# Performance work log

Measured on AMD Instinct MI355X. Metric: run time of the kernel, lower is better.

Reference implementation:

```python
import jax, jax.numpy as jnp
import numpy as np

B, S, D, MAX_CLS = 128, 512, 768, 64


def setup_inputs() -> dict:
    key = jax.random.key(0)
    k1, k2 = jax.random.split(key)
    encoded_output = jax.random.normal(k1, (B, S, D), dtype=jnp.float32)
    W = jax.random.normal(k2, (D, 1), dtype=jnp.float32) * 0.02
    b = jnp.zeros((1,), dtype=jnp.float32)
    # Build cls_idx with a variable number of CLS positions per row;
    # row 0 gets exactly MAX_CLS so the batch max equals MAX_CLS (matches
    # the original data-dependent max(cls_idx.sum(dim=1))).
    rng = np.random.default_rng(0)
    cls = np.zeros((B, S), dtype=bool)
    counts = rng.integers(8, MAX_CLS + 1, size=B)
    counts[0] = MAX_CLS
    for i in range(B):
        pos = rng.choice(S, size=counts[i], replace=False)
        cls[i, pos] = True
    cls_idx = jnp.asarray(cls)
    return {"encoded_output": encoded_output, "W": W, "b": b,
            "cls_idx": cls_idx, "max_num_cls": MAX_CLS}


def reference(encoded_output, W, b, cls_idx, max_num_cls):
    # extract_cls_embeddings: mask, ragged-gather CLS rows, pad to max count.
    maskf = cls_idx[..., None].astype(encoded_output.dtype)  # [B,S,1]
    masked = encoded_output * maskf                          # [B,S,D]
    # stable argsort puts True (CLS) positions first, preserving order
    order = jnp.argsort(jnp.logical_not(cls_idx), axis=1, stable=True)  # [B,S]
    idx = order[:, :max_num_cls]                             # [B,M]
    gathered = jnp.take_along_axis(masked, idx[..., None], axis=1)  # [B,M,D]
    counts = jnp.sum(cls_idx, axis=1)                        # [B]
    valid = jnp.arange(max_num_cls)[None, :] < counts[:, None]  # [B,M]
    gathered = gathered * valid[..., None].astype(gathered.dtype)  # zero-pad
    # LinearClassifier: linear + sigmoid
    logits = jax.nn.sigmoid(jnp.einsum('bmd,dk->bmk', gathered, W) + b)
    return logits
```

## Files before the change

### kernel.cpp

```cpp
#include <hip/hip_runtime.h>
#include <math.h>

#define B_  128
#define S_  512
#define D_  768
#define M_  64

__global__ void Summarizer_pos_kernel(const int* __restrict__ cls,
                                      int* __restrict__ pos,
                                      int* __restrict__ cnt) {
    const int b    = blockIdx.x;
    const int lane = threadIdx.x;
    const int* row = cls + (size_t)b * S_;

    int base = 0;
    #pragma unroll
    for (int i = 0; i < S_ / 64; ++i) {
        const int v = row[i * 64 + lane];
        const unsigned long long mask = __ballot(v != 0);
        const unsigned long long below = (lane == 0) ? 0ull
                                        : (mask & ((1ull << lane) - 1ull));
        const int rank = base + __popcll(below);
        if (v != 0 && rank < M_) {
            pos[(size_t)b * M_ + rank] = i * 64 + lane;
        }
        base += __popcll(mask);
    }
    if (lane == 0) cnt[b] = (base < M_) ? base : M_;
}

__global__ void Summarizer_dot_kernel(const float* __restrict__ enc,
                                      const float* __restrict__ W,
                                      const float* __restrict__ bias,
                                      const int* __restrict__ pos,
                                      const int* __restrict__ cnt,
                                      float* __restrict__ out) {
    const int tid  = blockIdx.x * blockDim.x + threadIdx.x;
    const int wid  = tid >> 6;
    const int lane = tid & 63;
    const int b    = wid >> 6;
    const int m    = wid & (M_ - 1);

    float sum = 0.0f;
    const int count = cnt[b];
    if (m < count) {
        const int p = pos[(size_t)b * M_ + m];
        const float4* row4 = (const float4*)(enc + ((size_t)b * S_ + p) * D_);
        const float4* w4   = (const float4*)W;

        const float4 r0 = row4[lane];
        const float4 r1 = row4[lane + 64];
        const float4 r2 = row4[lane + 128];
        const float4 w0 = w4[lane];
        const float4 w1 = w4[lane + 64];
        const float4 w2 = w4[lane + 128];

        sum = r0.x * w0.x + r0.y * w0.y + r0.z * w0.z + r0.w * w0.w
            + r1.x * w1.x + r1.y * w1.y + r1.z * w1.z + r1.w * w1.w
            + r2.x * w2.x + r2.y * w2.y + r2.z * w2.z + r2.w * w2.w;
    }

    #pragma unroll
    for (int off = 32; off > 0; off >>= 1) {
        sum += __shfl_down(sum, off, 64);
    }

    if (lane == 0) {
        const float x = sum + bias[0];
        out[wid] = 1.0f / (1.0f + __expf(-x));
    }
}

extern "C" void kernel_launch(void* const* d_in, const int* in_sizes, int n_in,
                              void* d_out, int out_size, void* d_ws, size_t ws_size,
                              hipStream_t stream) {
    const float* enc  = (const float*)d_in[0];
    const float* W    = (const float*)d_in[1];
    const float* bias = (const float*)d_in[2];
    const int*   cls  = (const int*)d_in[3];
    float* out = (float*)d_out;

    int* pos = (int*)d_ws;
    int* cnt = pos + (size_t)B_ * M_;

    Summarizer_pos_kernel<<<B_, 64, 0, stream>>>(cls, pos, cnt);

    const int total_threads = B_ * M_ * 64;
    Summarizer_dot_kernel<<<total_threads / 256, 256, 0, stream>>>(
        enc, W, bias, pos, cnt, out);
}
```

Baseline: 242.7 us.

## Fuse CLS position scan and dot-product into one kernel

```diff
diff --git a/kernel.cpp b/kernel.cpp
--- a/kernel.cpp
+++ b/kernel.cpp
@@ -6,68 +6,67 @@
 #define D_  768
 #define M_  64
 
-__global__ void Summarizer_pos_kernel(const int* __restrict__ cls,
-                                      int* __restrict__ pos,
-                                      int* __restrict__ cnt) {
-    const int b    = blockIdx.x;
-    const int lane = threadIdx.x;
-    const int* row = cls + (size_t)b * S_;
+__global__ __launch_bounds__(256) void Summarizer_fused_kernel(
+    const float* __restrict__ enc,
+    const float* __restrict__ W,
+    const float* __restrict__ bias,
+    const int*   __restrict__ cls,
+    float*       __restrict__ out) {
 
-    int base = 0;
-    #pragma unroll
-    for (int i = 0; i < S_ / 64; ++i) {
-        const int v = row[i * 64 + lane];
-        const unsigned long long mask = __ballot(v != 0);
-        const unsigned long long below = (lane == 0) ? 0ull
-                                        : (mask & ((1ull << lane) - 1ull));
-        const int rank = base + __popcll(below);
-        if (v != 0 && rank < M_) {
-            pos[(size_t)b * M_ + rank] = i * 64 + lane;
+    __shared__ int s_pos[M_];
+    __shared__ int s_cnt;
+
+    const int tid  = threadIdx.x;
+    const int lane = tid & 63;
+    const int wave = tid >> 6;
+    const int b    = blockIdx.x >> 1;
+    const int half = blockIdx.x & 1;
+
+    if (wave == 0) {
+        const int* row = cls + (size_t)b * S_;
+        int base = 0;
+        #pragma unroll
+        for (int i = 0; i < S_ / 64; ++i) {
+            const int v = row[i * 64 + lane];
+            const unsigned long long mask  = __ballot(v != 0);
+            const unsigned long long below = mask & ((1ull << lane) - 1ull);
+            const int rank = base + __popcll(below);
+            if (v != 0 && rank < M_) s_pos[rank] = i * 64 + lane;
+            base += __popcll(mask);
         }
-        base += __popcll(mask);
-    }
-    if (lane == 0) cnt[b] = (base < M_) ? base : M_;
-}
-
-__global__ void Summarizer_dot_kernel(const float* __restrict__ enc,
-                                      const float* __restrict__ W,
-                                      const float* __restrict__ bias,
-                                      const int* __restrict__ pos,
-                                      const int* __restrict__ cnt,
-                                      float* __restrict__ out) {
-    const int tid  = blockIdx.x * blockDim.x + threadIdx.x;
-    const int wid  = tid >> 6;
-    const int lane = tid & 63;
-    const int b    = wid >> 6;
-    const int m    = wid & (M_ - 1);
-
-    float sum = 0.0f;
-    const int count = cnt[b];
-    if (m < count) {
-        const int p = pos[(size_t)b * M_ + m];
-        const float4* row4 = (const float4*)(enc + ((size_t)b * S_ + p) * D_);
-        const float4* w4   = (const float4*)W;
-
-        const float4 r0 = row4[lane];
-        const float4 r1 = row4[lane + 64];
-        const float4 r2 = row4[lane + 128];
-        const float4 w0 = w4[lane];
-        const float4 w1 = w4[lane + 64];
-        const float4 w2 = w4[lane + 128];
-
-        sum = r0.x * w0.x + r0.y * w0.y + r0.z * w0.z + r0.w * w0.w
-            + r1.x * w1.x + r1.y * w1.y + r1.z * w1.z + r1.w * w1.w
-            + r2.x * w2.x + r2.y * w2.y + r2.z * w2.z + r2.w * w2.w;
+        if (lane == 0) s_cnt = (base < M_) ? base : M_;
     }
 
+    const float4* w4 = (const float4*)W;
+    const float4 w0 = w4[lane];
+    const float4 w1 = w4[lane + 64];
+    const float4 w2 = w4[lane + 128];
+    const float  bb = bias[0];
+
+    __syncthreads();
+    const int count = s_cnt;
+
     #pragma unroll
-    for (int off = 32; off > 0; off >>= 1) {
-        sum += __shfl_down(sum, off, 64);
-    }
-
-    if (lane == 0) {
-        const float x = sum + bias[0];
-        out[wid] = 1.0f / (1.0f + __expf(-x));
+    for (int it = 0; it < M_ / 8; ++it) {
+        const int m = half * (M_ / 2) + it * 4 + wave;
+        float sum = 0.0f;
+        if (m < count) {
+            const float4* row4 =
+                (const float4*)(enc + ((size_t)b * S_ + s_pos[m]) * D_);
+            const float4 r0 = row4[lane];
+            const float4 r1 = row4[lane + 64];
+            const float4 r2 = row4[lane + 128];
+            sum = r0.x * w0.x + r0.y * w0.y + r0.z * w0.z + r0.w * w0.w
+                + r1.x * w1.x + r1.y * w1.y + r1.z * w1.z + r1.w * w1.w
+                + r2.x * w2.x + r2.y * w2.y + r2.z * w2.z + r2.w * w2.w;
+        }
+        #pragma unroll
+        for (int off = 32; off > 0; off >>= 1) {
+            sum += __shfl_down(sum, off, 64);
+        }
+        if (lane == 0) {
+            out[(size_t)b * M_ + m] = 1.0f / (1.0f + __expf(-(sum + bb)));
+        }
     }
 }
 
@@ -78,14 +77,8 @@
     const float* W    = (const float*)d_in[1];
     const float* bias = (const float*)d_in[2];
     const int*   cls  = (const int*)d_in[3];
+
     float* out = (float*)d_out;
 
-    int* pos = (int*)d_ws;
-    int* cnt = pos + (size_t)B_ * M_;
-
-    Summarizer_pos_kernel<<<B_, 64, 0, stream>>>(cls, pos, cnt);
-
-    const int total_threads = B_ * M_ * 64;
-    Summarizer_dot_kernel<<<total_threads / 256, 256, 0, stream>>>(
-        enc, W, bias, pos, cnt, out);
+    Summarizer_fused_kernel<<<B_ * 2, 256, 0, stream>>>(enc, W, bias, cls, out);
 }
```

Result: no change. 240.8 us (-0.8%).
